# Kernel tuning notes

Hardware: AMD Instinct MI355X
Metric: run time of the kernel (lower is better)

## Reference

```python
import jax, jax.numpy as jnp
import numpy as np

DEPTH = 8
HID = 512
EXP = 4
EPS = 1e-5


def setup_inputs() -> dict:
    key = jax.random.key(0)
    ks = jax.random.split(key, 12)
    B = 131072
    x = jax.random.normal(ks[0], (B, HID), dtype=jnp.float32)
    # input projection (input_dim=HID -> hidden_dim=HID)
    W_in = jax.random.normal(ks[1], (HID, HID), dtype=jnp.float32) * (1.0 / HID)
    b_in = jnp.zeros((HID,), dtype=jnp.float32)
    # stacked per-block params [DEPTH, ...]
    ln_g = jnp.ones((DEPTH, HID), dtype=jnp.float32)
    ln_b = jnp.zeros((DEPTH, HID), dtype=jnp.float32)
    W1 = jax.random.normal(ks[2], (DEPTH, HID, EXP), dtype=jnp.float32) * (1.0 / EXP)
    b1 = jnp.zeros((DEPTH, EXP), dtype=jnp.float32)
    W2 = jax.random.normal(ks[3], (DEPTH, EXP, HID), dtype=jnp.float32) * (1.0 / HID)
    b2 = jnp.zeros((DEPTH, HID), dtype=jnp.float32)
    # head (hidden_dim -> output_dim=HID)
    W_head = jax.random.normal(ks[4], (HID, HID), dtype=jnp.float32) * (1.0 / HID)
    b_head = jnp.zeros((HID,), dtype=jnp.float32)
    return {"x": x, "W_in": W_in, "b_in": b_in, "ln_g": ln_g, "ln_b": ln_b,
            "W1": W1, "b1": b1, "W2": W2, "b2": b2,
            "W_head": W_head, "b_head": b_head}


def _layernorm(x, g, b):
    mu = jnp.mean(x, axis=-1, keepdims=True)
    var = jnp.mean(jnp.square(x - mu), axis=-1, keepdims=True)
    return (x - mu) * jax.lax.rsqrt(var + EPS) * g + b


def reference(x, W_in, b_in, ln_g, ln_b, W1, b1, W2, b2, W_head, b_head):
    # mlp_input: Linear + relu (dropout=0.0 -> identity)
    h = jax.nn.relu(x @ W_in + b_in)  # [B, HID]

    def block(h, p):
        g, bb, w1, bb1, w2, bb2 = p
        z = _layernorm(h, g, bb)
        z = jax.nn.relu(z @ w1 + bb1)  # [B, EXP]
        z = z @ w2 + bb2               # [B, HID]
        return h + z, None

    h, _ = jax.lax.scan(block, h, (ln_g, ln_b, W1, b1, W2, b2))
    return h @ W_head + b_head
```

## Files before the change

kernel.cpp:

```cpp
#include <hip/hip_runtime.h>
#include <cstdint>

typedef unsigned short u16;
typedef unsigned int   u32;
typedef float  f32x4  __attribute__((ext_vector_type(4)));
typedef short  short8 __attribute__((ext_vector_type(8)));

__device__ inline float bf2f(u16 b){ u32 u=((u32)b)<<16; float f; __builtin_memcpy(&f,&u,4); return f; }
__device__ inline u16 f2bf(float f){ u32 u; __builtin_memcpy(&u,&f,4); u32 r=u+0x7FFFu+((u>>16)&1u); return (u16)(r>>16); }
__device__ inline u32 pk(float hi, float lo){ u32 a,b; __builtin_memcpy(&a,&hi,4); __builtin_memcpy(&b,&lo,4); return __builtin_amdgcn_perm(a,b,0x07060302u); }
__device__ inline u32 pkr(float hi, float lo){ return (u32)f2bf(lo) | ((u32)f2bf(hi)<<16); }
__device__ inline void gload_lds16(const void* g, void* l){
  __builtin_amdgcn_global_load_lds((const __attribute__((address_space(1))) unsigned int*)g,
                                   (__attribute__((address_space(3))) unsigned int*)l, 16, 0, 0);
}

__global__ __launch_bounds__(256) void prep_k(
    const float* __restrict__ W_in, const float* __restrict__ W_head,
    const float* __restrict__ ln_g, const float* __restrict__ W1,
    const float* __restrict__ W2, const float* __restrict__ b2,
    u16* __restrict__ Wt_in3, u16* __restrict__ Wt_hd3,
    u16* __restrict__ gw1f, u16* __restrict__ updA)
{
  int idx = blockIdx.x * 256 + threadIdx.x;
  if (idx < 524288){
    int which = idx >> 18;
    int q = idx & 262143;
    int t = q >> 14, o = q & 16383;
    int line = o >> 6, w = o & 63, slot = w >> 3, i = w & 7;
    int c8 = slot ^ (line & 7);
    int n = 2 * line + (c8 >> 2);
    int g = c8 & 3;
    if (which == 0){
      int k = t * 32 + g * 8 + i;
      Wt_in3[q] = f2bf(W_in[k * 512 + n]);
    } else {
      int k = t * 32 + (i < 4 ? 4 * g + i : 12 + 4 * g + i);
      Wt_hd3[q] = f2bf(W_head[k * 512 + n]);
    }
  } else if (idx < 544768){
    int q = idx - 524288;
    int d = q / 2560, r = q % 2560;
    int c = r / 160, r2 = r % 160;
    int g = r2 / 40, r3 = r2 % 40;
    int col = r3 >> 3, i = r3 & 7;
    int k = 32 * c + (i < 4 ? 4 * g + i : 12 + 4 * g + i);
    u16 v;
    if (col == 4) v = 0x3F80u;
    else          v = f2bf(ln_g[d * 512 + k] * W1[(d * 512 + k) * 4 + col]);
    gw1f[q] = v;
  } else if (idx < 577536){
    int q = idx - 544768;
    int d = q >> 12, r = q & 4095;
    int t = r >> 7, r2 = r & 127;
    int m = r2 >> 3, sl = r2 & 7;
    int k = 16 * t + m;
    u16 v = 0;
    if (sl < 4)       v = f2bf(W2[(d * 4 + sl) * 512 + k]);
    else if (sl == 4) v = f2bf(b2[d * 512 + k]);
    updA[q] = v;
  }
}

__global__ __launch_bounds__(64) void uv_k(
    const float* __restrict__ ln_g, const float* __restrict__ ln_b,
    const float* __restrict__ W1, const float* __restrict__ b1,
    float* __restrict__ U, float* __restrict__ V)
{
  int d = blockIdx.x >> 2, e = blockIdx.x & 3;
  int lane = threadIdx.x;
  float u = 0.f, v = 0.f;
  for (int k = lane; k < 512; k += 64){
    float w = W1[(d * 512 + k) * 4 + e];
    u += bf2f(f2bf(ln_g[d * 512 + k] * w));
    v += ln_b[d * 512 + k] * w;
  }
  for (int m = 1; m < 64; m <<= 1){ u += __shfl_xor(u, m); v += __shfl_xor(v, m); }
  if (lane == 0){ U[d * 4 + e] = u; V[d * 4 + e] = v + b1[d * 4 + e]; }
}

__global__ __launch_bounds__(512, 2) void fused_k(
    const float* __restrict__ x, const u16* __restrict__ Wt_in3,
    const float* __restrict__ b_in, const u16* __restrict__ Wt_hd3,
    const float* __restrict__ b_head, const u16* __restrict__ gw1f,
    const u16* __restrict__ updA, const float* __restrict__ U,
    const float* __restrict__ V, float* __restrict__ out)
{
  __shared__ __align__(16) char LT[96544];
  constexpr int HX = 65536, SSo = 81920, ZBo = 94208, UVo = 96256, SZo = 96512;
  float* sSf = (float*)(LT + SSo);
  float* zbf = (float*)(LT + ZBo);
  float* sUV = (float*)(LT + UVo);
  u16*   sZ  = (u16*)(LT + SZo);

  const int tid  = threadIdx.x;
  const int wv   = tid >> 6;
  const int lane = tid & 63;
  const int m    = lane & 15;
  const int g    = lane >> 4;
  const int nq   = wv & 3;
  const int rh   = wv >> 2;
  const size_t rowbase = (size_t)blockIdx.x * 128 + rh * 64;

  if (tid < 32) sUV[tid] = U[tid];
  else if (tid < 64) sUV[tid] = V[tid - 32];
  if (tid >= 64 && tid < 72) sZ[tid - 64] = 0;

  auto stageA = [&](const u16* W, int t, char* dst){
    const char* src = (const char*)(W + t * 16384) + tid * 16;
    char* d2 = dst + tid * 16;
    #pragma unroll
    for (int j = 0; j < 4; ++j)
      gload_lds16(src + j * 8192, d2 + j * 8192);
  };
  auto stageM = [&](int d, int bf2){
    char* dsg = LT + 32768 + bf2 * 16384;
    if (tid < 320)
      gload_lds16((const char*)gw1f + d * 5120 + tid * 16, dsg + tid * 16);
    gload_lds16((const char*)updA + d * 8192 + tid * 16, dsg + 5120 + tid * 16);
  };

  auto mkfrag = [&](f32x4 a, f32x4 b)->short8{
    union{u32 u[4]; short8 s;} t;
    t.u[0]=pkr(a[1],a[0]); t.u[1]=pkr(a[3],a[2]);
    t.u[2]=pkr(b[1],b[0]); t.u[3]=pkr(b[3],b[2]);
    return t.s;
  };
  auto mkfragT = [&](f32x4 a, f32x4 b)->short8{
    union{u32 u[4]; short8 s;} t;
    t.u[0]=pk(a[1],a[0]); t.u[1]=pk(a[3],a[2]);
    t.u[2]=pk(b[1],b[0]); t.u[3]=pk(b[3],b[2]);
    return t.s;
  };

  const int afoff = (m >> 1) * 128 + (((((m & 1) << 2) | g) ^ ((m >> 1) & 7)) << 4);

  f32x4 hv[4][4][2];
  #pragma unroll
  for (int q = 0; q < 4; ++q)
    #pragma unroll
    for (int c2 = 0; c2 < 4; ++c2){ hv[q][c2][0] = (f32x4)0.f; hv[q][c2][1] = (f32x4)0.f; }

  const float* xbase = x + (rowbase + m) * 512 + g * 8;
  short8 bq[2][4];
  {
    f32x4 x0[4][2];
    #pragma unroll
    for (int q = 0; q < 4; ++q){
      x0[q][0] = *(const f32x4*)(xbase + q * 8192);
      x0[q][1] = *(const f32x4*)(xbase + q * 8192 + 4);
    }
    stageA(Wt_in3, 0, LT);
    #pragma unroll
    for (int q = 0; q < 4; ++q) bq[0][q] = mkfrag(x0[q][0], x0[q][1]);
  }
  __syncthreads();

  #pragma unroll 2
  for (int t = 0; t < 16; ++t){
    const int pb = t & 1;
    if (t < 15) stageA(Wt_in3, t + 1, LT + ((t + 1) & 1) * 32768);
    f32x4 xn[4][2];
    if (t < 15){
      #pragma unroll
      for (int q = 0; q < 4; ++q){
        xn[q][0] = *(const f32x4*)(xbase + q * 8192 + (t + 1) * 32);
        xn[q][1] = *(const f32x4*)(xbase + q * 8192 + (t + 1) * 32 + 4);
      }
    }
    const char* wb = LT + pb * 32768 + nq * 8192 + afoff;
    #pragma unroll
    for (int f = 0; f < 8; ++f){
      short8 aw = *(const short8*)(wb + f * 1024);
      #pragma unroll
      for (int q = 0; q < 4; ++q)
        hv[q][f >> 1][f & 1] =
          __builtin_amdgcn_mfma_f32_16x16x32_bf16(aw, bq[pb][q], hv[q][f >> 1][f & 1], 0, 0, 0);
    }
    if (t < 15){
      #pragma unroll
      for (int q = 0; q < 4; ++q) bq[pb ^ 1][q] = mkfrag(xn[q][0], xn[q][1]);
    }
    __syncthreads();
  }

  #pragma unroll
  for (int q = 0; q < 4; ++q)
    #pragma unroll
    for (int c2 = 0; c2 < 4; ++c2)
      #pragma unroll
      for (int hf = 0; hf < 2; ++hf){
        f32x4 bi = *(const f32x4*)(b_in + nq * 128 + c2 * 32 + hf * 16 + g * 4);
        #pragma unroll
        for (int r = 0; r < 4; ++r){
          float v = hv[q][c2][hf][r] + bi[r];
          v = v > 0.f ? v : 0.f;
          hv[q][c2][hf][r] = bf2f(f2bf(v));
        }
      }

  stageM(0, 0);
  __syncthreads();
  int buf = 0;
  #pragma unroll 1
  for (int d = 0; d < 8; ++d){
    if (d < 7) stageM(d + 1, buf ^ 1);
    else       stageA(Wt_hd3, 0, LT);

    const u16* sGp = (const u16*)(LT + 32768 + buf * 16384);
    const u16* sAp = sGp + 2560;

    const u16* gb = (m < 5) ? (sGp + nq * 640 + g * 40 + m * 8) : sZ;
    const int gstep = (m < 5) ? 160 : 0;
    f32x4 aS[4], aG[4];
    #pragma unroll
    for (int q = 0; q < 4; ++q){ aS[q] = (f32x4)0.f; aG[q] = (f32x4)0.f; }
    #pragma unroll
    for (int c2 = 0; c2 < 4; ++c2){
      short8 bf = *(const short8*)(gb + c2 * gstep);
      #pragma unroll
      for (int q = 0; q < 4; ++q){
        short8 af = mkfragT(hv[q][c2][0], hv[q][c2][1]);
        aS[q] = __builtin_amdgcn_mfma_f32_16x16x32_bf16(af, bf, aS[q], 0, 0, 0);
        aG[q] = __builtin_amdgcn_mfma_f32_16x16x32_bf16(af, af, aG[q], 0, 0, 0);
      }
    }

    #pragma unroll
    for (int q = 0; q < 4; ++q){
      if (m < 5)
        *(f32x4*)(sSf + (((rh * 4 + q) * 4 + nq) * 6 + m) * 16 + 4 * g) = aS[q];
      if ((m >> 2) == g)
        sSf[(((rh * 4 + q) * 4 + nq) * 6 + 5) * 16 + m] = aG[q][m & 3];
    }
    __syncthreads();

    if (tid < 128){
      int rh2 = tid >> 6, rl = tid & 63, q2 = rl >> 4, b = rl & 15;
      float S0 = 0.f, S1 = 0.f, S2 = 0.f, S3 = 0.f, sm = 0.f, sq = 0.f;
      #pragma unroll
      for (int nn = 0; nn < 4; ++nn){
        const float* pp = sSf + (((rh2 * 4 + q2) * 4 + nn) * 6) * 16 + b;
        S0 += pp[0]; S1 += pp[16]; S2 += pp[32]; S3 += pp[48];
        sm += pp[64]; sq += pp[80];
      }
      float mu  = sm * (1.f / 512.f);
      float var = sq * (1.f / 512.f) - mu * mu;
      float rs  = rsqrtf(var + 1e-5f);
      f32x4 zz;
      float z0 = fmaf(rs, S0 - mu * sUV[d * 4 + 0], sUV[32 + d * 4 + 0]);
      float z1 = fmaf(rs, S1 - mu * sUV[d * 4 + 1], sUV[32 + d * 4 + 1]);
      float z2 = fmaf(rs, S2 - mu * sUV[d * 4 + 2], sUV[32 + d * 4 + 2]);
      float z3 = fmaf(rs, S3 - mu * sUV[d * 4 + 3], sUV[32 + d * 4 + 3]);
      zz[0] = z0 > 0.f ? z0 : 0.f;
      zz[1] = z1 > 0.f ? z1 : 0.f;
      zz[2] = z2 > 0.f ? z2 : 0.f;
      zz[3] = z3 > 0.f ? z3 : 0.f;
      *(f32x4*)(zbf + tid * 4) = zz;
    }
    __syncthreads();

    #pragma unroll
    for (int q = 0; q < 4; ++q){
      f32x4 z4 = *(const f32x4*)(zbf + (rh * 64 + q * 16 + m) * 4);
      union{u32 u[4]; short8 s;} bz;
      bz.u[0] = (g == 0) ? pk(z4[1], z4[0]) : 0u;
      bz.u[1] = (g == 0) ? pk(z4[3], z4[2]) : 0u;
      bz.u[2] = (g == 0) ? 0x00003F80u : 0u;
      bz.u[3] = 0u;
      const u16* ab = (g == 0) ? (sAp + nq * 1024 + m * 8) : sZ;
      const int ainc = (g == 0) ? 128 : 0;
      #pragma unroll
      for (int t2 = 0; t2 < 8; ++t2){
        short8 aw = *(const short8*)(ab + t2 * ainc);
        hv[q][t2 >> 1][t2 & 1] =
          __builtin_amdgcn_mfma_f32_16x16x32_bf16(aw, bz.s, hv[q][t2 >> 1][t2 & 1], 0, 0, 0);
      }
    }
    __syncthreads();
    buf ^= 1;
  }

  short8 p[4][4];
  #pragma unroll
  for (int q = 0; q < 4; ++q)
    #pragma unroll
    for (int c2 = 0; c2 < 4; ++c2)
      p[q][c2] = mkfrag(hv[q][c2][0], hv[q][c2][1]);

  f32x4 acc[4][8];
  #pragma unroll
  for (int q = 0; q < 4; ++q)
    #pragma unroll
    for (int of = 0; of < 8; ++of) acc[q][of] = (f32x4)0.f;

  if (nq == 0){
    #pragma unroll
    for (int q = 0; q < 4; ++q)
      *(short8*)(LT + HX + rh * 4096 + (q * 64 + m * 4 + g) * 16) = p[q][0];
  }
  __syncthreads();

  #pragma unroll 4
  for (int c = 0; c < 16; ++c){
    if (c < 15){
      stageA(Wt_hd3, c + 1, LT + ((c + 1) & 1) * 32768);
      if (nq == ((c + 1) >> 2)){
        #pragma unroll
        for (int q = 0; q < 4; ++q)
          *(short8*)(LT + HX + ((c + 1) & 1) * 8192 + rh * 4096 + (q * 64 + m * 4 + g) * 16)
            = p[q][(c + 1) & 3];
      }
    }
    const char* hxb = LT + HX + (c & 1) * 8192 + rh * 4096 + (m * 4 + g) * 16;
    short8 bh[4];
    #pragma unroll
    for (int q = 0; q < 4; ++q) bh[q] = *(const short8*)(hxb + q * 1024);
    const char* wb = LT + (c & 1) * 32768 + nq * 8192 + afoff;
    #pragma unroll
    for (int of = 0; of < 8; ++of){
      short8 aw = *(const short8*)(wb + of * 1024);
      #pragma unroll
      for (int q = 0; q < 4; ++q)
        acc[q][of] = __builtin_amdgcn_mfma_f32_16x16x32_bf16(aw, bh[q], acc[q][of], 0, 0, 0);
    }
    __syncthreads();
  }

  #pragma unroll
  for (int q = 0; q < 4; ++q)
    #pragma unroll
    for (int of = 0; of < 8; ++of){
      f32x4 bhd = *(const f32x4*)(b_head + nq * 128 + of * 16 + g * 4);
      f32x4 v;
      #pragma unroll
      for (int r = 0; r < 4; ++r) v[r] = acc[q][of][r] + bhd[r];
      *(f32x4*)(out + (rowbase + q * 16 + m) * 512 + nq * 128 + of * 16 + g * 4) = v;
    }
}

extern "C" void kernel_launch(void* const* d_in, const int* in_sizes, int n_in,
                              void* d_out, int out_size, void* d_ws, size_t ws_size,
                              hipStream_t stream)
{
  const float* x      = (const float*)d_in[0];
  const float* W_in   = (const float*)d_in[1];
  const float* b_in   = (const float*)d_in[2];
  const float* ln_g   = (const float*)d_in[3];
  const float* ln_b   = (const float*)d_in[4];
  const float* W1     = (const float*)d_in[5];
  const float* b1     = (const float*)d_in[6];
  const float* W2     = (const float*)d_in[7];
  const float* b2     = (const float*)d_in[8];
  const float* W_head = (const float*)d_in[9];
  const float* b_head = (const float*)d_in[10];
  float* out = (float*)d_out;
  const int B = in_sizes[0] / 512;

  char* ws = (char*)d_ws;
  u16*   Wt_in3 = (u16*)ws;
  u16*   Wt_hd3 = Wt_in3 + 262144;
  u16*   gw1f   = Wt_hd3 + 262144;
  u16*   updA   = gw1f + 20480;
  float* Up     = (float*)(updA + 32768);
  float* Vp     = Up + 32;

  prep_k<<<2256, 256, 0, stream>>>(W_in, W_head, ln_g, W1, W2, b2, Wt_in3, Wt_hd3, gw1f, updA);
  uv_k<<<32, 64, 0, stream>>>(ln_g, ln_b, W1, b1, Up, Vp);
  fused_k<<<B / 128, 512, 0, stream>>>(x, Wt_in3, b_in, Wt_hd3, b_head, gw1f, updA, Up, Vp, out);
}
```

Measured before the change: 397.8 us.

## Triple-buffer weight staging with partial vmcnt barriers in input and head GEMMs

Moves the input-projection and head GEMM weight tiles from double to triple buffering in LDS, prefetching two tiles ahead. Full __syncthreads waits are replaced by barriers that wait only until the older loads have landed (partial vmcnt), so later prefetches stay in flight. The x prefetch is also deepened to two stages held in registers, and both loops are fully unrolled. The cost is more LDS (about 131KB, likely dropping occupancy from 2 blocks/CU to 1) and more register pressure, and the hand-set vmcnt counts must match the number of issued loads exactly.

```diff
diff --git a/kernel.cpp b/kernel.cpp
--- a/kernel.cpp
+++ b/kernel.cpp
@@ -14,6 +14,9 @@
   __builtin_amdgcn_global_load_lds((const __attribute__((address_space(1))) unsigned int*)g,
                                    (__attribute__((address_space(3))) unsigned int*)l, 16, 0, 0);
 }
+
+#define CBAR(K) do{ asm volatile("s_waitcnt vmcnt(" #K ") lgkmcnt(0)" ::: "memory"); \
+  __builtin_amdgcn_s_barrier(); __builtin_amdgcn_sched_barrier(0); }while(0)
 
 __global__ __launch_bounds__(256) void prep_k(
     const float* __restrict__ W_in, const float* __restrict__ W_head,
@@ -86,8 +89,10 @@
     const u16* __restrict__ updA, const float* __restrict__ U,
     const float* __restrict__ V, float* __restrict__ out)
 {
-  __shared__ __align__(16) char LT[96544];
-  constexpr int HX = 65536, SSo = 81920, ZBo = 94208, UVo = 96256, SZo = 96512;
+  __shared__ __align__(16) char LT[131344];
+  constexpr int SSo = 65536, ZBo = 77824;
+  constexpr int MIDB = 98304, HXo = 98304;
+  constexpr int UVo = 131072, SZo = 131328;
   float* sSf = (float*)(LT + SSo);
   float* zbf = (float*)(LT + ZBo);
   float* sUV = (float*)(LT + UVo);
@@ -114,7 +119,7 @@
       gload_lds16(src + j * 8192, d2 + j * 8192);
   };
   auto stageM = [&](int d, int bf2){
-    char* dsg = LT + 32768 + bf2 * 16384;
+    char* dsg = LT + MIDB + bf2 * 16384;
     if (tid < 320)
       gload_lds16((const char*)gw1f + d * 5120 + tid * 16, dsg + tid * 16);
     gload_lds16((const char*)updA + d * 8192 + tid * 16, dsg + 5120 + tid * 16);
@@ -142,46 +147,48 @@
     for (int c2 = 0; c2 < 4; ++c2){ hv[q][c2][0] = (f32x4)0.f; hv[q][c2][1] = (f32x4)0.f; }
 
   const float* xbase = x + (rowbase + m) * 512 + g * 8;
-  short8 bq[2][4];
-  {
-    f32x4 x0[4][2];
-    #pragma unroll
-    for (int q = 0; q < 4; ++q){
-      x0[q][0] = *(const f32x4*)(xbase + q * 8192);
-      x0[q][1] = *(const f32x4*)(xbase + q * 8192 + 4);
-    }
-    stageA(Wt_in3, 0, LT);
-    #pragma unroll
-    for (int q = 0; q < 4; ++q) bq[0][q] = mkfrag(x0[q][0], x0[q][1]);
-  }
+  f32x4 xA[4][2], xB[4][2];
+  #pragma unroll
+  for (int q = 0; q < 4; ++q){
+    xA[q][0] = *(const f32x4*)(xbase + q * 8192);
+    xA[q][1] = *(const f32x4*)(xbase + q * 8192 + 4);
+    xB[q][0] = *(const f32x4*)(xbase + q * 8192 + 32);
+    xB[q][1] = *(const f32x4*)(xbase + q * 8192 + 36);
+  }
+  stageA(Wt_in3, 0, LT);
+  stageA(Wt_in3, 1, LT + 32768);
   __syncthreads();
 
-  #pragma unroll 2
+  #pragma unroll
   for (int t = 0; t < 16; ++t){
-    const int pb = t & 1;
-    if (t < 15) stageA(Wt_in3, t + 1, LT + ((t + 1) & 1) * 32768);
-    f32x4 xn[4][2];
-    if (t < 15){
+    if (t < 14) stageA(Wt_in3, t + 2, LT + ((t + 2) % 3) * 32768);
+    short8 bq[4];
+    #pragma unroll
+    for (int q = 0; q < 4; ++q)
+      bq[q] = (t & 1) ? mkfrag(xB[q][0], xB[q][1]) : mkfrag(xA[q][0], xA[q][1]);
+    if (t < 14){
       #pragma unroll
       for (int q = 0; q < 4; ++q){
-        xn[q][0] = *(const f32x4*)(xbase + q * 8192 + (t + 1) * 32);
-        xn[q][1] = *(const f32x4*)(xbase + q * 8192 + (t + 1) * 32 + 4);
-      }
-    }
-    const char* wb = LT + pb * 32768 + nq * 8192 + afoff;
+        if (t & 1){
+          xB[q][0] = *(const f32x4*)(xbase + q * 8192 + (t + 2) * 32);
+          xB[q][1] = *(const f32x4*)(xbase + q * 8192 + (t + 2) * 32 + 4);
+        } else {
+          xA[q][0] = *(const f32x4*)(xbase + q * 8192 + (t + 2) * 32);
+          xA[q][1] = *(const f32x4*)(xbase + q * 8192 + (t + 2) * 32 + 4);
+        }
+      }
+    }
+    const char* wb = LT + (t % 3) * 32768 + nq * 8192 + afoff;
     #pragma unroll
     for (int f = 0; f < 8; ++f){
       short8 aw = *(const short8*)(wb + f * 1024);
       #pragma unroll
       for (int q = 0; q < 4; ++q)
         hv[q][f >> 1][f & 1] =
-          __builtin_amdgcn_mfma_f32_16x16x32_bf16(aw, bq[pb][q], hv[q][f >> 1][f & 1], 0, 0, 0);
-    }
-    if (t < 15){
-      #pragma unroll
-      for (int q = 0; q < 4; ++q) bq[pb ^ 1][q] = mkfrag(xn[q][0], xn[q][1]);
-    }
-    __syncthreads();
+          __builtin_amdgcn_mfma_f32_16x16x32_bf16(aw, bq[q], hv[q][f >> 1][f & 1], 0, 0, 0);
+    }
+    if (t < 14)       CBAR(20);
+    else if (t == 14) CBAR(8);
   }
 
   #pragma unroll
@@ -207,7 +214,7 @@
     if (d < 7) stageM(d + 1, buf ^ 1);
     else       stageA(Wt_hd3, 0, LT);
 
-    const u16* sGp = (const u16*)(LT + 32768 + buf * 16384);
+    const u16* sGp = (const u16*)(LT + MIDB + buf * 16384);
     const u16* sAp = sGp + 2560;
 
     const u16* gb = (m < 5) ? (sGp + nq * 640 + g * 40 + m * 8) : sZ;
@@ -297,26 +304,25 @@
   if (nq == 0){
     #pragma unroll
     for (int q = 0; q < 4; ++q)
-      *(short8*)(LT + HX + rh * 4096 + (q * 64 + m * 4 + g) * 16) = p[q][0];
-  }
+      *(short8*)(LT + HXo + rh * 4096 + (q * 64 + m * 4 + g) * 16) = p[q][0];
+  }
+  stageA(Wt_hd3, 1, LT + 32768);
   __syncthreads();
 
-  #pragma unroll 4
+  #pragma unroll
   for (int c = 0; c < 16; ++c){
-    if (c < 15){
-      stageA(Wt_hd3, c + 1, LT + ((c + 1) & 1) * 32768);
-      if (nq == ((c + 1) >> 2)){
-        #pragma unroll
-        for (int q = 0; q < 4; ++q)
-          *(short8*)(LT + HX + ((c + 1) & 1) * 8192 + rh * 4096 + (q * 64 + m * 4 + g) * 16)
-            = p[q][(c + 1) & 3];
-      }
-    }
-    const char* hxb = LT + HX + (c & 1) * 8192 + rh * 4096 + (m * 4 + g) * 16;
+    if (c < 14) stageA(Wt_hd3, c + 2, LT + ((c + 2) % 3) * 32768);
+    if (c < 15 && nq == ((c + 1) >> 2)){
+      #pragma unroll
+      for (int q = 0; q < 4; ++q)
+        *(short8*)(LT + HXo + ((c + 1) & 1) * 8192 + rh * 4096 + (q * 64 + m * 4 + g) * 16)
+          = p[q][(c + 1) & 3];
+    }
+    const char* hxb = LT + HXo + (c & 1) * 8192 + rh * 4096 + (m * 4 + g) * 16;
     short8 bh[4];
     #pragma unroll
     for (int q = 0; q < 4; ++q) bh[q] = *(const short8*)(hxb + q * 1024);
-    const char* wb = LT + (c & 1) * 32768 + nq * 8192 + afoff;
+    const char* wb = LT + (c % 3) * 32768 + nq * 8192 + afoff;
     #pragma unroll
     for (int of = 0; of < 8; ++of){
       short8 aw = *(const short8*)(wb + of * 1024);
@@ -324,7 +330,8 @@
       for (int q = 0; q < 4; ++q)
         acc[q][of] = __builtin_amdgcn_mfma_f32_16x16x32_bf16(aw, bh[q], acc[q][of], 0, 0, 0);
     }
-    __syncthreads();
+    if (c < 14)       CBAR(4);
+    else if (c == 14) CBAR(0);
   }
 
   #pragma unroll
```

Result: faster. 365.0 us (-8.2%).

## Shrink fused block to 64 rows and use fine-grained vmcnt barriers

Applied to the files above, without the earlier changes.

Halves the workgroup to 256 threads covering 64 rows, which shrinks LDS to 80KB so more workgroups can share a CU, and doubles the grid. Full __syncthreads are replaced with s_waitcnt vmcnt(N) plus s_barrier so the next weight tile's async loads stay in flight across the barrier. Float-to-bf16 conversions switch to the hardware v_cvt_pk_bf16_f32 instruction. The cost is that each block now reloads all weights for half as many rows, doubling weight traffic into LDS, and the hand-tuned wait counts must exactly match the number of outstanding loads.

```diff
diff --git a/kernel.cpp b/kernel.cpp
--- a/kernel.cpp
+++ b/kernel.cpp
@@ -8,12 +8,16 @@
 
 __device__ inline float bf2f(u16 b){ u32 u=((u32)b)<<16; float f; __builtin_memcpy(&f,&u,4); return f; }
 __device__ inline u16 f2bf(float f){ u32 u; __builtin_memcpy(&u,&f,4); u32 r=u+0x7FFFu+((u>>16)&1u); return (u16)(r>>16); }
+__device__ inline float ubits(u32 u){ float f; __builtin_memcpy(&f,&u,4); return f; }
 __device__ inline u32 pk(float hi, float lo){ u32 a,b; __builtin_memcpy(&a,&hi,4); __builtin_memcpy(&b,&lo,4); return __builtin_amdgcn_perm(a,b,0x07060302u); }
-__device__ inline u32 pkr(float hi, float lo){ return (u32)f2bf(lo) | ((u32)f2bf(hi)<<16); }
+__device__ inline u32 cvtpk(float lo, float hi){ u32 r; asm("v_cvt_pk_bf16_f32 %0, %1, %2" : "=v"(r) : "v"(lo), "v"(hi)); return r; }
 __device__ inline void gload_lds16(const void* g, void* l){
   __builtin_amdgcn_global_load_lds((const __attribute__((address_space(1))) unsigned int*)g,
                                    (__attribute__((address_space(3))) unsigned int*)l, 16, 0, 0);
 }
+
+#define CBAR(K) do{ asm volatile("s_waitcnt vmcnt(" #K ") lgkmcnt(0)" ::: "memory"); \
+  __builtin_amdgcn_s_barrier(); __builtin_amdgcn_sched_barrier(0); }while(0)
 
 __global__ __launch_bounds__(256) void prep_k(
     const float* __restrict__ W_in, const float* __restrict__ W_head,
@@ -79,28 +83,28 @@
   if (lane == 0){ U[d * 4 + e] = u; V[d * 4 + e] = v + b1[d * 4 + e]; }
 }
 
-__global__ __launch_bounds__(512, 2) void fused_k(
+__global__ __launch_bounds__(256, 2) void fused_k(
     const float* __restrict__ x, const u16* __restrict__ Wt_in3,
     const float* __restrict__ b_in, const u16* __restrict__ Wt_hd3,
     const float* __restrict__ b_head, const u16* __restrict__ gw1f,
     const u16* __restrict__ updA, const float* __restrict__ U,
     const float* __restrict__ V, float* __restrict__ out)
 {
-  __shared__ __align__(16) char LT[96544];
-  constexpr int HX = 65536, SSo = 81920, ZBo = 94208, UVo = 96256, SZo = 96512;
+  __shared__ __align__(16) char LT[81920];
+  constexpr int MIDB = 32768;
+  constexpr int HXo  = 65536;
+  constexpr int SSo  = 73728, ZBo = 79872, UVo = 80896, SZo = 81152;
   float* sSf = (float*)(LT + SSo);
   float* zbf = (float*)(LT + ZBo);
   float* sUV = (float*)(LT + UVo);
   u16*   sZ  = (u16*)(LT + SZo);
 
   const int tid  = threadIdx.x;
-  const int wv   = tid >> 6;
   const int lane = tid & 63;
   const int m    = lane & 15;
   const int g    = lane >> 4;
-  const int nq   = wv & 3;
-  const int rh   = wv >> 2;
-  const size_t rowbase = (size_t)blockIdx.x * 128 + rh * 64;
+  const int nq   = tid >> 6;
+  const size_t rowbase = (size_t)blockIdx.x * 64;
 
   if (tid < 32) sUV[tid] = U[tid];
   else if (tid < 64) sUV[tid] = V[tid - 32];
@@ -110,20 +114,23 @@
     const char* src = (const char*)(W + t * 16384) + tid * 16;
     char* d2 = dst + tid * 16;
     #pragma unroll
-    for (int j = 0; j < 4; ++j)
-      gload_lds16(src + j * 8192, d2 + j * 8192);
+    for (int j = 0; j < 8; ++j)
+      gload_lds16(src + j * 4096, d2 + j * 4096);
   };
   auto stageM = [&](int d, int bf2){
-    char* dsg = LT + 32768 + bf2 * 16384;
-    if (tid < 320)
-      gload_lds16((const char*)gw1f + d * 5120 + tid * 16, dsg + tid * 16);
-    gload_lds16((const char*)updA + d * 8192 + tid * 16, dsg + 5120 + tid * 16);
+    char* dsg = LT + MIDB + bf2 * 13312;
+    const char* gs = (const char*)gw1f + d * 5120;
+    gload_lds16(gs + tid * 16, dsg + tid * 16);
+    if (tid < 64) gload_lds16(gs + 4096 + tid * 16, dsg + 4096 + tid * 16);
+    const char* as = (const char*)updA + d * 8192;
+    gload_lds16(as + tid * 16, dsg + 5120 + tid * 16);
+    gload_lds16(as + 4096 + tid * 16, dsg + 5120 + 4096 + tid * 16);
   };
 
   auto mkfrag = [&](f32x4 a, f32x4 b)->short8{
     union{u32 u[4]; short8 s;} t;
-    t.u[0]=pkr(a[1],a[0]); t.u[1]=pkr(a[3],a[2]);
-    t.u[2]=pkr(b[1],b[0]); t.u[3]=pkr(b[3],b[2]);
+    t.u[0]=cvtpk(a[0],a[1]); t.u[1]=cvtpk(a[2],a[3]);
+    t.u[2]=cvtpk(b[0],b[1]); t.u[3]=cvtpk(b[2],b[3]);
     return t.s;
   };
   auto mkfragT = [&](f32x4 a, f32x4 b)->short8{
@@ -142,47 +149,40 @@
     for (int c2 = 0; c2 < 4; ++c2){ hv[q][c2][0] = (f32x4)0.f; hv[q][c2][1] = (f32x4)0.f; }
 
   const float* xbase = x + (rowbase + m) * 512 + g * 8;
-  short8 bq[2][4];
-  {
-    f32x4 x0[4][2];
-    #pragma unroll
-    for (int q = 0; q < 4; ++q){
-      x0[q][0] = *(const f32x4*)(xbase + q * 8192);
-      x0[q][1] = *(const f32x4*)(xbase + q * 8192 + 4);
-    }
-    stageA(Wt_in3, 0, LT);
-    #pragma unroll
-    for (int q = 0; q < 4; ++q) bq[0][q] = mkfrag(x0[q][0], x0[q][1]);
-  }
+  f32x4 xv[4][2];
+  #pragma unroll
+  for (int q = 0; q < 4; ++q){
+    xv[q][0] = *(const f32x4*)(xbase + q * 8192);
+    xv[q][1] = *(const f32x4*)(xbase + q * 8192 + 4);
+  }
+  stageA(Wt_in3, 0, LT);
   __syncthreads();
 
   #pragma unroll 2
   for (int t = 0; t < 16; ++t){
-    const int pb = t & 1;
     if (t < 15) stageA(Wt_in3, t + 1, LT + ((t + 1) & 1) * 32768);
-    f32x4 xn[4][2];
+    short8 bq[4];
+    #pragma unroll
+    for (int q = 0; q < 4; ++q) bq[q] = mkfrag(xv[q][0], xv[q][1]);
     if (t < 15){
       #pragma unroll
       for (int q = 0; q < 4; ++q){
-        xn[q][0] = *(const f32x4*)(xbase + q * 8192 + (t + 1) * 32);
-        xn[q][1] = *(const f32x4*)(xbase + q * 8192 + (t + 1) * 32 + 4);
-      }
-    }
-    const char* wb = LT + pb * 32768 + nq * 8192 + afoff;
+        xv[q][0] = *(const f32x4*)(xbase + q * 8192 + (t + 1) * 32);
+        xv[q][1] = *(const f32x4*)(xbase + q * 8192 + (t + 1) * 32 + 4);
+      }
+    }
+    const char* wb = LT + (t & 1) * 32768 + nq * 8192 + afoff;
     #pragma unroll
     for (int f = 0; f < 8; ++f){
       short8 aw = *(const short8*)(wb + f * 1024);
       #pragma unroll
       for (int q = 0; q < 4; ++q)
         hv[q][f >> 1][f & 1] =
-          __builtin_amdgcn_mfma_f32_16x16x32_bf16(aw, bq[pb][q], hv[q][f >> 1][f & 1], 0, 0, 0);
-    }
-    if (t < 15){
-      #pragma unroll
-      for (int q = 0; q < 4; ++q) bq[pb ^ 1][q] = mkfrag(xn[q][0], xn[q][1]);
-    }
-    __syncthreads();
-  }
+          __builtin_amdgcn_mfma_f32_16x16x32_bf16(aw, bq[q], hv[q][f >> 1][f & 1], 0, 0, 0);
+    }
+    if (t < 15) CBAR(8);
+  }
+  __syncthreads();
 
   #pragma unroll
   for (int q = 0; q < 4; ++q)
@@ -191,23 +191,26 @@
       #pragma unroll
       for (int hf = 0; hf < 2; ++hf){
         f32x4 bi = *(const f32x4*)(b_in + nq * 128 + c2 * 32 + hf * 16 + g * 4);
+        f32x4 v;
         #pragma unroll
-        for (int r = 0; r < 4; ++r){
-          float v = hv[q][c2][hf][r] + bi[r];
-          v = v > 0.f ? v : 0.f;
-          hv[q][c2][hf][r] = bf2f(f2bf(v));
-        }
+        for (int r = 0; r < 4; ++r){ float w = hv[q][c2][hf][r] + bi[r]; v[r] = w > 0.f ? w : 0.f; }
+        u32 ua = cvtpk(v[0], v[1]), ub = cvtpk(v[2], v[3]);
+        hv[q][c2][hf][0] = ubits(ua << 16);
+        hv[q][c2][hf][1] = ubits(ua & 0xFFFF0000u);
+        hv[q][c2][hf][2] = ubits(ub << 16);
+        hv[q][c2][hf][3] = ubits(ub & 0xFFFF0000u);
       }
 
   stageM(0, 0);
   __syncthreads();
+
   int buf = 0;
   #pragma unroll 1
   for (int d = 0; d < 8; ++d){
     if (d < 7) stageM(d + 1, buf ^ 1);
     else       stageA(Wt_hd3, 0, LT);
 
-    const u16* sGp = (const u16*)(LT + 32768 + buf * 16384);
+    const u16* sGp = (const u16*)(LT + MIDB + buf * 13312);
     const u16* sAp = sGp + 2560;
 
     const u16* gb = (m < 5) ? (sGp + nq * 640 + g * 40 + m * 8) : sZ;
@@ -229,18 +232,18 @@
     #pragma unroll
     for (int q = 0; q < 4; ++q){
       if (m < 5)
-        *(f32x4*)(sSf + (((rh * 4 + q) * 4 + nq) * 6 + m) * 16 + 4 * g) = aS[q];
+        *(f32x4*)(sSf + ((q * 4 + nq) * 6 + m) * 16 + 4 * g) = aS[q];
       if ((m >> 2) == g)
-        sSf[(((rh * 4 + q) * 4 + nq) * 6 + 5) * 16 + m] = aG[q][m & 3];
-    }
-    __syncthreads();
-
-    if (tid < 128){
-      int rh2 = tid >> 6, rl = tid & 63, q2 = rl >> 4, b = rl & 15;
+        sSf[((q * 4 + nq) * 6 + 5) * 16 + m] = aG[q][m & 3];
+    }
+    CBAR(8);
+
+    if (tid < 64){
+      int q2 = tid >> 4, b = tid & 15;
       float S0 = 0.f, S1 = 0.f, S2 = 0.f, S3 = 0.f, sm = 0.f, sq = 0.f;
       #pragma unroll
       for (int nn = 0; nn < 4; ++nn){
-        const float* pp = sSf + (((rh2 * 4 + q2) * 4 + nn) * 6) * 16 + b;
+        const float* pp = sSf + ((q2 * 4 + nn) * 6) * 16 + b;
         S0 += pp[0]; S1 += pp[16]; S2 += pp[32]; S3 += pp[48];
         sm += pp[64]; sq += pp[80];
       }
@@ -258,11 +261,11 @@
       zz[3] = z3 > 0.f ? z3 : 0.f;
       *(f32x4*)(zbf + tid * 4) = zz;
     }
-    __syncthreads();
+    CBAR(8);
 
     #pragma unroll
     for (int q = 0; q < 4; ++q){
-      f32x4 z4 = *(const f32x4*)(zbf + (rh * 64 + q * 16 + m) * 4);
+      f32x4 z4 = *(const f32x4*)(zbf + (q * 16 + m) * 4);
       union{u32 u[4]; short8 s;} bz;
       bz.u[0] = (g == 0) ? pk(z4[1], z4[0]) : 0u;
       bz.u[1] = (g == 0) ? pk(z4[3], z4[2]) : 0u;
@@ -297,22 +300,21 @@
   if (nq == 0){
     #pragma unroll
     for (int q = 0; q < 4; ++q)
-      *(short8*)(LT + HX + rh * 4096 + (q * 64 + m * 4 + g) * 16) = p[q][0];
-  }
-  __syncthreads();
-
-  #pragma unroll 4
+      *(short8*)(LT + HXo + (q * 64 + m * 4 + g) * 16) = p[q][0];
+  }
+  stageA(Wt_hd3, 1, LT + 32768);
+  CBAR(8);
+
+  #pragma unroll 2
   for (int c = 0; c < 16; ++c){
-    if (c < 15){
-      stageA(Wt_hd3, c + 1, LT + ((c + 1) & 1) * 32768);
-      if (nq == ((c + 1) >> 2)){
-        #pragma unroll
-        for (int q = 0; q < 4; ++q)
-          *(short8*)(LT + HX + ((c + 1) & 1) * 8192 + rh * 4096 + (q * 64 + m * 4 + g) * 16)
-            = p[q][(c + 1) & 3];
-      }
-    }
-    const char* hxb = LT + HX + (c & 1) * 8192 + rh * 4096 + (m * 4 + g) * 16;
+    if (c >= 1 && c < 15) stageA(Wt_hd3, c + 1, LT + ((c + 1) & 1) * 32768);
+    if (c < 15 && nq == ((c + 1) >> 2)){
+      #pragma unroll
+      for (int q = 0; q < 4; ++q)
+        *(short8*)(LT + HXo + ((c + 1) & 1) * 4096 + (q * 64 + m * 4 + g) * 16)
+          = p[q][(c + 1) & 3];
+    }
+    const char* hxb = LT + HXo + (c & 1) * 4096 + (m * 4 + g) * 16;
     short8 bh[4];
     #pragma unroll
     for (int q = 0; q < 4; ++q) bh[q] = *(const short8*)(hxb + q * 1024);
@@ -324,7 +326,7 @@
       for (int q = 0; q < 4; ++q)
         acc[q][of] = __builtin_amdgcn_mfma_f32_16x16x32_bf16(aw, bh[q], acc[q][of], 0, 0, 0);
     }
-    __syncthreads();
+    if (c < 15) CBAR(0);
   }
 
   #pragma unroll
@@ -367,5 +369,5 @@
 
   prep_k<<<2256, 256, 0, stream>>>(W_in, W_head, ln_g, W1, W2, b2, Wt_in3, Wt_hd3, gw1f, updA);
   uv_k<<<32, 64, 0, stream>>>(ln_g, ln_b, W1, b1, Up, Vp);
-  fused_k<<<B / 128, 512, 0, stream>>>(x, Wt_in3, b_in, Wt_hd3, b_head, gw1f, updA, Up, Vp, out);
-}
+  fused_k<<<B / 64, 256, 0, stream>>>(x, Wt_in3, b_in, Wt_hd3, b_head, gw1f, updA, Up, Vp, out);
+}
```

Result: faster. 384.1 us (-3.4%).
